# Performance work log

Hardware: AMD Instinct MI355X
Metric: run time of the kernel (lower is better)

## Reference

```python
import jax, jax.numpy as jnp
import numpy as np

B, T, C = 4, 1024, 1024
HS = 64                 # head_size_a
H = C // HS             # 16 heads
H_KV = 4                # num_key_value_heads
N_REP = H // H_KV       # GQA repeat factor
D_DECAY = 64            # max(32, round(1.8*sqrt(1024)/32)*32)
D_MV = 32               # max(32, round(1.3*sqrt(1024)/32)*32)
LAYER_ID = 1
N_LAYER = 24
EPS = 0.00064


def setup_inputs() -> dict:
    key = jax.random.key(0)
    ks = jax.random.split(key, 16)
    def nrm(k, shape, s):
        return jax.random.normal(k, shape, jnp.float32) * s
    ratio_0_to_1 = LAYER_ID / (N_LAYER - 1)
    n = np.arange(C, dtype=np.float64)
    decay_speed = -7.0 + 5.0 * (n / (C - 1)) ** (0.85 + 1.0 * ratio_0_to_1 ** 0.5)
    return dict(
        x=nrm(ks[0], (B, T, C), 1.0),
        v_first=nrm(ks[1], (B, T, C), 1.0),
        attention_mask=jnp.ones((B, T), jnp.float32),
        Wr=nrm(ks[2], (H * HS, C), C ** -0.5),
        Wk=nrm(ks[3], (H_KV * HS, C), C ** -0.5),
        Wv=nrm(ks[4], (H_KV * HS, C), C ** -0.5),
        Wo=nrm(ks[5], (C, H * HS), C ** -0.5),
        w0=jnp.asarray(decay_speed + 0.5, jnp.float32),
        w1=nrm(ks[6], (C, D_DECAY), 0.02),
        w2=nrm(ks[7], (D_DECAY, C), 0.02),
        a0=jnp.zeros((C,), jnp.float32),
        a1=nrm(ks[8], (C, D_DECAY), 0.02),
        a2=nrm(ks[9], (D_DECAY, C), 0.02),
        v0=jnp.ones((C,), jnp.float32),
        v1=nrm(ks[10], (C, D_MV), 0.02),
        v2=nrm(ks[11], (D_MV, C), 0.02),
        k_k=jnp.full((C,), 0.85, jnp.float32),
        k_a=jnp.ones((C,), jnp.float32),
        r_k=nrm(ks[12], (H, HS), 0.02),
        ln_g=jnp.ones((C,), jnp.float32),
        ln_b=jnp.zeros((C,), jnp.float32),
    )


def _wkv7(r, w, k, v, a, b, mask):
    """RWKV-7 delta-rule recurrence. r,w,k,v,a,b: (B,T,C); mask: (B,T).
    State S: (B,H,N_value,N_key). Per step:
      S = S * exp(-exp(w)) + (S @ a) b^T + v k^T ;  y = S @ r
    """
    Bx, Tx, Cx = r.shape
    def rs(t):  # (B,T,C) -> (T,B,H,N)
        return t.reshape(Bx, Tx, H, HS).transpose(1, 0, 2, 3)
    decay = jnp.exp(-jnp.exp(w))
    m = mask.T[:, :, None, None]  # (T,B,1,1)
    rT, dT, kT, vT, aT, bT = map(rs, (r, decay, k, v, a, b))
    kT = kT * m; vT = vT * m; aT = aT * m; bT = bT * m
    dT = jnp.where(m > 0, dT, 1.0)  # masked steps leave state untouched

    def step(S, inp):
        r_t, d_t, k_t, v_t, a_t, b_t = inp  # each (B,H,N)
        sa = jnp.einsum('bhij,bhj->bhi', S, a_t)
        S = S * d_t[:, :, None, :] + sa[..., None] * b_t[:, :, None, :] \
            + v_t[..., None] * k_t[:, :, None, :]
        y = jnp.einsum('bhij,bhj->bhi', S, r_t)
        return S, y

    S0 = jnp.zeros((Bx, H, HS, HS), r.dtype)
    _, yT = jax.lax.scan(step, S0, (rT, dT, kT, vT, aT, bT))
    return yT.transpose(1, 0, 2, 3).reshape(Bx, Tx, Cx)


def reference(x, v_first, attention_mask, Wr, Wk, Wv, Wo, w0, w1, w2,
              a0, a1, a2, v0, v1, v2, k_k, k_a, r_k, ln_g, ln_b):
    B_, T_, C_ = x.shape
    r = x @ Wr.T
    w = -jax.nn.softplus(-(w0 + jnp.tanh(x @ w1) @ w2)) - 0.6
    k = x @ Wk.T  # (B,T,H_KV*HS)
    v = x @ Wv.T

    def rep(t):  # GQA repeat_kv: (B,T,H_kv*N) -> (B,T,H*N)
        t = t.reshape(B_, T_, H_KV, 1, HS)
        return jnp.broadcast_to(t, (B_, T_, H_KV, N_REP, HS)).reshape(B_, T_, C_)
    k = rep(k); v = rep(v)

    # layer_id != 0: residual mix with first layer's v
    v = v + (v_first - v) * jax.nn.sigmoid(v0 + x @ v1 @ v2)
    a = jax.nn.sigmoid(a0 + x @ a1 @ a2)

    kk = (k * k_k).reshape(B_, T_, H, HS)
    kk = kk / jnp.maximum(jnp.linalg.norm(kk, axis=-1, keepdims=True), 1e-12)
    kk = kk.reshape(B_, T_, C_)
    k = k * (1.0 + (a - 1.0) * k_a)

    y = _wkv7(r, w, k, v, -kk, kk * a, attention_mask)

    # GroupNorm(H, C): per-head normalization over HS channels
    yh = y.reshape(B_, T_, H, HS)
    mu = yh.mean(-1, keepdims=True)
    var = yh.var(-1, keepdims=True)
    y = ((yh - mu) / jnp.sqrt(var + EPS)).reshape(B_, T_, C_) * ln_g + ln_b

    rk = (r.reshape(B_, T_, H, HS) * k.reshape(B_, T_, H, HS) * r_k).sum(-1, keepdims=True)
    y = y + (rk * v.reshape(B_, T_, H, HS)).reshape(B_, T_, C_)
    out = y @ Wo.T
    return (out, v_first)
```

## Files before the change

### kernel.cpp

```cpp
#include <hip/hip_runtime.h>


#define NROWS 4096
#define CCH   1024
#define EPSV  0.00064f

typedef __attribute__((ext_vector_type(4))) float f32x4;
typedef __attribute__((ext_vector_type(8))) short bf16x8;

__device__ __forceinline__ unsigned short f2b(float f) {
    unsigned x = __float_as_uint(f);
    return (unsigned short)((x + 0x7fffu + ((x >> 16) & 1u)) >> 16);
}
__device__ __forceinline__ float b2f(unsigned short u) {
    return __uint_as_float(((unsigned)u) << 16);
}

#define LDSTR 40

template<bool TANH>
__global__ __launch_bounds__(256) void gemm_split(
    const float* __restrict__ A, int lda, const float* __restrict__ B, int ldb,
    float* __restrict__ C, int ldc, int M, int N, int K, int tl, int th)
{
    __shared__ __align__(16) unsigned short Ah[128 * LDSTR];
    __shared__ __align__(16) unsigned short Al[128 * LDSTR];
    __shared__ __align__(16) unsigned short Bh[128 * LDSTR];
    __shared__ __align__(16) unsigned short Bl[128 * LDSTR];
    const int t = threadIdx.x;
    const int wave = t >> 6, lane = t & 63;
    const int m0 = blockIdx.y * 128, n0 = blockIdx.x * 128;
    const int wm = (wave >> 1) * 64, wn = (wave & 1) * 64;
    const int fr = lane & 15, kq = lane >> 4;

    f32x4 acc[4][4];
    #pragma unroll
    for (int i = 0; i < 4; ++i)
        #pragma unroll
        for (int j = 0; j < 4; ++j)
            acc[i][j] = (f32x4){0.f, 0.f, 0.f, 0.f};

    const int srow = t >> 3;
    const int scol = (t & 7) * 4;

    for (int k0 = 0; k0 < K; k0 += 32) {
        #pragma unroll
        for (int p = 0; p < 4; ++p) {
            const int row = p * 32 + srow;
            {
                const float4 v = *reinterpret_cast<const float4*>(
                    A + (size_t)(m0 + row) * lda + k0 + scol);
                ushort4 h, l;
                h.x = f2b(v.x); l.x = f2b(v.x - b2f(h.x));
                h.y = f2b(v.y); l.y = f2b(v.y - b2f(h.y));
                h.z = f2b(v.z); l.z = f2b(v.z - b2f(h.z));
                h.w = f2b(v.w); l.w = f2b(v.w - b2f(h.w));
                *reinterpret_cast<ushort4*>(&Ah[row * LDSTR + scol]) = h;
                *reinterpret_cast<ushort4*>(&Al[row * LDSTR + scol]) = l;
            }
            {
                float4 v = make_float4(0.f, 0.f, 0.f, 0.f);
                if (n0 + row < N)
                    v = *reinterpret_cast<const float4*>(
                        B + (size_t)(n0 + row) * ldb + k0 + scol);
                ushort4 h, l;
                h.x = f2b(v.x); l.x = f2b(v.x - b2f(h.x));
                h.y = f2b(v.y); l.y = f2b(v.y - b2f(h.y));
                h.z = f2b(v.z); l.z = f2b(v.z - b2f(h.z));
                h.w = f2b(v.w); l.w = f2b(v.w - b2f(h.w));
                *reinterpret_cast<ushort4*>(&Bh[row * LDSTR + scol]) = h;
                *reinterpret_cast<ushort4*>(&Bl[row * LDSTR + scol]) = l;
            }
        }
        __syncthreads();

        bf16x8 ah[4], al[4], bh[4], bl[4];
        #pragma unroll
        for (int mi = 0; mi < 4; ++mi) {
            ah[mi] = *reinterpret_cast<const bf16x8*>(&Ah[(wm + mi * 16 + fr) * LDSTR + kq * 8]);
            al[mi] = *reinterpret_cast<const bf16x8*>(&Al[(wm + mi * 16 + fr) * LDSTR + kq * 8]);
        }
        #pragma unroll
        for (int ni = 0; ni < 4; ++ni) {
            bh[ni] = *reinterpret_cast<const bf16x8*>(&Bh[(wn + ni * 16 + fr) * LDSTR + kq * 8]);
            bl[ni] = *reinterpret_cast<const bf16x8*>(&Bl[(wn + ni * 16 + fr) * LDSTR + kq * 8]);
        }
        #pragma unroll
        for (int mi = 0; mi < 4; ++mi)
            #pragma unroll
            for (int ni = 0; ni < 4; ++ni) {
                acc[mi][ni] = __builtin_amdgcn_mfma_f32_16x16x32_bf16(
                    al[mi], bh[ni], acc[mi][ni], 0, 0, 0);
                acc[mi][ni] = __builtin_amdgcn_mfma_f32_16x16x32_bf16(
                    ah[mi], bl[ni], acc[mi][ni], 0, 0, 0);
                acc[mi][ni] = __builtin_amdgcn_mfma_f32_16x16x32_bf16(
                    ah[mi], bh[ni], acc[mi][ni], 0, 0, 0);
            }
        __syncthreads();
    }

    const int crow0 = m0 + wm + kq * 4;
    const int ccol0 = n0 + wn + fr;
    #pragma unroll
    for (int mi = 0; mi < 4; ++mi)
        #pragma unroll
        for (int ni = 0; ni < 4; ++ni) {
            const int col = ccol0 + ni * 16;
            if (col < N) {
                #pragma unroll
                for (int i = 0; i < 4; ++i) {
                    float v = acc[mi][ni][i];
                    if (TANH && col >= tl && col < th) v = tanhf(v);
                    C[(size_t)(crow0 + mi * 16 + i) * ldc + col] = v;
                }
            }
        }
}

__global__ __launch_bounds__(256) void gemm_mfma(
    const float* __restrict__ A, int lda, const float* __restrict__ B, int ldb,
    float* __restrict__ C, int ldc, int M, int N, int K)
{
    __shared__ __align__(16) unsigned short Ah[128 * LDSTR];
    __shared__ __align__(16) unsigned short Bh[128 * LDSTR];
    const int t = threadIdx.x;
    const int wave = t >> 6, lane = t & 63;
    const int m0 = blockIdx.y * 128, n0 = blockIdx.x * 128;
    const int wm = (wave >> 1) * 64, wn = (wave & 1) * 64;
    const int fr = lane & 15, kq = lane >> 4;

    f32x4 acc[4][4];
    #pragma unroll
    for (int i = 0; i < 4; ++i)
        #pragma unroll
        for (int j = 0; j < 4; ++j)
            acc[i][j] = (f32x4){0.f, 0.f, 0.f, 0.f};

    const int srow = t >> 3;
    const int scol = (t & 7) * 4;

    for (int k0 = 0; k0 < K; k0 += 32) {
        #pragma unroll
        for (int p = 0; p < 4; ++p) {
            const int row = p * 32 + srow;
            const float4 av = *reinterpret_cast<const float4*>(
                A + (size_t)(m0 + row) * lda + k0 + scol);
            ushort4 a4;
            a4.x = f2b(av.x); a4.y = f2b(av.y); a4.z = f2b(av.z); a4.w = f2b(av.w);
            *reinterpret_cast<ushort4*>(&Ah[row * LDSTR + scol]) = a4;
            const float4 bv = *reinterpret_cast<const float4*>(
                B + (size_t)(n0 + row) * ldb + k0 + scol);
            ushort4 b4;
            b4.x = f2b(bv.x); b4.y = f2b(bv.y); b4.z = f2b(bv.z); b4.w = f2b(bv.w);
            *reinterpret_cast<ushort4*>(&Bh[row * LDSTR + scol]) = b4;
        }
        __syncthreads();

        bf16x8 af[4], bfr[4];
        #pragma unroll
        for (int mi = 0; mi < 4; ++mi)
            af[mi] = *reinterpret_cast<const bf16x8*>(&Ah[(wm + mi * 16 + fr) * LDSTR + kq * 8]);
        #pragma unroll
        for (int ni = 0; ni < 4; ++ni)
            bfr[ni] = *reinterpret_cast<const bf16x8*>(&Bh[(wn + ni * 16 + fr) * LDSTR + kq * 8]);
        #pragma unroll
        for (int mi = 0; mi < 4; ++mi)
            #pragma unroll
            for (int ni = 0; ni < 4; ++ni)
                acc[mi][ni] = __builtin_amdgcn_mfma_f32_16x16x32_bf16(
                    af[mi], bfr[ni], acc[mi][ni], 0, 0, 0);
        __syncthreads();
    }

    const int crow0 = m0 + wm + kq * 4;
    const int ccol0 = n0 + wn + fr;
    #pragma unroll
    for (int mi = 0; mi < 4; ++mi)
        #pragma unroll
        for (int ni = 0; ni < 4; ++ni) {
            const int col = ccol0 + ni * 16;
            #pragma unroll
            for (int i = 0; i < 4; ++i)
                C[(size_t)(crow0 + mi * 16 + i) * ldc + col] = acc[mi][ni][i];
        }
}

__global__ __launch_bounds__(256) void gemm_stage2(
    const float* __restrict__ kvh,
    const float* __restrict__ w2T, const float* __restrict__ a2T,
    const float* __restrict__ v2T,
    float* __restrict__ wdec, float* __restrict__ kf, float* __restrict__ vf)
{
    const int z = blockIdx.z;
    const float* A = kvh + (z == 0 ? 512 : z == 1 ? 576 : 640);
    const float* B = z == 0 ? w2T : z == 1 ? a2T : v2T;
    float* C       = z == 0 ? wdec : z == 1 ? kf : vf;
    const int K    = z == 2 ? 32 : 64;
    const int ldb  = K;

    __shared__ __align__(16) unsigned short Ah[128 * LDSTR];
    __shared__ __align__(16) unsigned short Bh[128 * LDSTR];
    const int t = threadIdx.x;
    const int wave = t >> 6, lane = t & 63;
    const int m0 = blockIdx.y * 128, n0 = blockIdx.x * 128;
    const int wm = (wave >> 1) * 64, wn = (wave & 1) * 64;
    const int fr = lane & 15, kq = lane >> 4;

    f32x4 acc[4][4];
    #pragma unroll
    for (int i = 0; i < 4; ++i)
        #pragma unroll
        for (int j = 0; j < 4; ++j)
            acc[i][j] = (f32x4){0.f, 0.f, 0.f, 0.f};

    const int srow = t >> 3;
    const int scol = (t & 7) * 4;

    for (int k0 = 0; k0 < K; k0 += 32) {
        #pragma unroll
        for (int p = 0; p < 4; ++p) {
            const int row = p * 32 + srow;
            const float4 av = *reinterpret_cast<const float4*>(
                A + (size_t)(m0 + row) * 672 + k0 + scol);
            ushort4 a4;
            a4.x = f2b(av.x); a4.y = f2b(av.y); a4.z = f2b(av.z); a4.w = f2b(av.w);
            *reinterpret_cast<ushort4*>(&Ah[row * LDSTR + scol]) = a4;
            const float4 bv = *reinterpret_cast<const float4*>(
                B + (size_t)(n0 + row) * ldb + k0 + scol);
            ushort4 b4;
            b4.x = f2b(bv.x); b4.y = f2b(bv.y); b4.z = f2b(bv.z); b4.w = f2b(bv.w);
            *reinterpret_cast<ushort4*>(&Bh[row * LDSTR + scol]) = b4;
        }
        __syncthreads();

        bf16x8 af[4], bfr[4];
        #pragma unroll
        for (int mi = 0; mi < 4; ++mi)
            af[mi] = *reinterpret_cast<const bf16x8*>(&Ah[(wm + mi * 16 + fr) * LDSTR + kq * 8]);
        #pragma unroll
        for (int ni = 0; ni < 4; ++ni)
            bfr[ni] = *reinterpret_cast<const bf16x8*>(&Bh[(wn + ni * 16 + fr) * LDSTR + kq * 8]);
        #pragma unroll
        for (int mi = 0; mi < 4; ++mi)
            #pragma unroll
            for (int ni = 0; ni < 4; ++ni)
                acc[mi][ni] = __builtin_amdgcn_mfma_f32_16x16x32_bf16(
                    af[mi], bfr[ni], acc[mi][ni], 0, 0, 0);
        __syncthreads();
    }

    const int crow0 = m0 + wm + kq * 4;
    const int ccol0 = n0 + wn + fr;
    #pragma unroll
    for (int mi = 0; mi < 4; ++mi)
        #pragma unroll
        for (int ni = 0; ni < 4; ++ni) {
            const int col = ccol0 + ni * 16;
            #pragma unroll
            for (int i = 0; i < 4; ++i)
                C[(size_t)(crow0 + mi * 16 + i) * 1024 + col] = acc[mi][ni][i];
        }
}

__global__ __launch_bounds__(256) void pack_all(
    const float* __restrict__ Wk, const float* __restrict__ Wv,
    const float* __restrict__ w1, const float* __restrict__ a1,
    const float* __restrict__ v1, const float* __restrict__ w2,
    const float* __restrict__ a2, const float* __restrict__ v2,
    float* __restrict__ Wkvh,
    float* __restrict__ w2T, float* __restrict__ a2T, float* __restrict__ v2T)
{
    const int blk = blockIdx.x, t = threadIdx.x;
    if (blk < 512) {
        const float* s = blk < 256 ? Wk + (size_t)blk * 1024
                                   : Wv + (size_t)(blk - 256) * 1024;
        const float4 v = *reinterpret_cast<const float4*>(s + t * 4);
        *reinterpret_cast<float4*>(Wkvh + (size_t)blk * 1024 + t * 4) = v;
    } else if (blk < 672) {
        const int f = blk - 512;
        for (int c = t; c < 1024; c += 256) {
            float val;
            if (f < 64)       val = w1[c * 64 + f];
            else if (f < 128) val = a1[c * 64 + (f - 64)];
            else              val = v1[c * 32 + (f - 128)];
            Wkvh[(size_t)(512 + f) * 1024 + c] = val;
        }
    } else {
        const int c = blk - 672;
        if (t < 64)       w2T[c * 64 + t]         = w2[t * 1024 + c];
        else if (t < 128) a2T[c * 64 + (t - 64)]  = a2[(t - 64) * 1024 + c];
        else if (t < 160) v2T[c * 32 + (t - 128)] = v2[(t - 128) * 1024 + c];
    }
}

__global__ __launch_bounds__(256) void fuse_pre(
    const float* __restrict__ kvh,
    const float* __restrict__ v_first, const float* __restrict__ mask,
    const float* __restrict__ w0, const float* __restrict__ a0,
    const float* __restrict__ v0,
    const float* __restrict__ k_k, const float* __restrict__ k_a,
    float* __restrict__ wdec, float* __restrict__ kf, float* __restrict__ vf,
    float* __restrict__ aab, float* __restrict__ bbb)
{
    const int n = blockIdx.x, t = threadIdx.x;
    const float m = mask[n];
    const bool live = m > 0.f;

    #pragma unroll
    for (int q = 0; q < 4; ++q) {
        const int c = q * 256 + t;
        const size_t idx = (size_t)n * 1024 + c;
        const float dd   = w0[c] + wdec[idx];
        const float aacc = a0[c] + kf[idx];
        const float vacc = v0[c] + vf[idx];

        const float u  = -dd;
        const float sp = fmaxf(u, 0.f) + log1pf(expf(-fabsf(u)));
        const float dec = expf(-expf(-sp - 0.6f));
        const float av = 1.f / (1.f + expf(-aacc));
        const float sv = 1.f / (1.f + expf(-vacc));

        const int  ck  = q * 64 + (c & 63);
        const float kr = kvh[(size_t)n * 672 + ck];
        const float vr = kvh[(size_t)n * 672 + 256 + ck];
        const float vfi = v_first[idx];
        const float vv  = vr + (vfi - vr) * sv;

        const float tkk = kr * k_k[c];
        float ss = tkk * tkk;
        #pragma unroll
        for (int off = 32; off > 0; off >>= 1) ss += __shfl_xor(ss, off, 64);
        const float kkv = tkk / fmaxf(sqrtf(ss), 1e-12f);

        wdec[idx] = live ? dec : 1.f;
        kf[idx]   = kr * (1.f + (av - 1.f) * k_a[c]) * m;
        vf[idx]   = vv * m;
        aab[idx]  = -kkv * m;
        bbb[idx]  = kkv * av * m;
    }
}

__device__ __forceinline__ float qred16(float x) {
    x += __int_as_float(__builtin_amdgcn_update_dpp(
        0, __float_as_int(x), 0xB1, 0xF, 0xF, true));
    x += __int_as_float(__builtin_amdgcn_update_dpp(
        0, __float_as_int(x), 0x4E, 0xF, 0xF, true));
    x += __int_as_float(__builtin_amdgcn_update_dpp(
        0, __float_as_int(x), 0x141, 0xF, 0xF, true));
    x += __int_as_float(__builtin_amdgcn_update_dpp(
        0, __float_as_int(x), 0x140, 0xF, 0xF, true));
    return x;
}

__global__ __launch_bounds__(256, 1) void wkv7(
    const float* __restrict__ r, const float* __restrict__ wdec,
    const float* __restrict__ kf, const float* __restrict__ vf,
    const float* __restrict__ aab, const float* __restrict__ bbb,
    float* __restrict__ y)
{
    __shared__ __align__(16) float4 sl[2][672];
    const int blk = blockIdx.x;
    const int m  = blk & 7;
    const int s_ = blk >> 3;
    const int bh = (s_ >> 2) * 8 + m;
    const int j  = s_ & 3;
    const int b = bh >> 4, h = bh & 15;
    const int tid  = threadIdx.x;
    const int wave = tid >> 6;
    const int lane = tid & 63;
    const int li   = lane & 15;
    const int il   = wave * 4 + (lane >> 4);
    const int i    = j * 16 + il;
    const size_t cb = (size_t)b * (1024 * 1024) + (size_t)h * 64;

#define GLL16(g, l) __builtin_amdgcn_global_load_lds( \
        (const __attribute__((address_space(1))) unsigned int*)(g), \
        (__attribute__((address_space(3))) unsigned int*)(l), 16, 0, 0)

    auto stage = [&](int t0, int bf) {
        #pragma unroll
        for (int k = 0; k < 3; ++k) {
            const int q = tid + k * 256;
            if (q < 672) {
                const float* gp;
                if (q < 640) {
                    const int s  = q / 80;
                    const int rm = q - s * 80;
                    const int arr = rm >> 4, c16 = rm & 15;
                    const float* base = arr == 0 ? wdec : arr == 1 ? kf
                                      : arr == 2 ? aab : arr == 3 ? bbb : r;
                    gp = base + cb + (size_t)(t0 + s) * 1024 + c16 * 4;
                } else {
                    const int qq = q - 640;
                    const int s = qq >> 2, c4 = qq & 3;
                    gp = vf + cb + (size_t)(t0 + s) * 1024 + j * 16 + c4 * 4;
                }
                GLL16(gp, &sl[bf][wave * 64 + k * 256]);
            }
        }
    };

    float4 S = (float4){0.f, 0.f, 0.f, 0.f};

    stage(0, 0);
    asm volatile("s_waitcnt vmcnt(0)" ::: "memory");
    __builtin_amdgcn_sched_barrier(0);
    __builtin_amdgcn_s_barrier();

    for (int g = 0; g < 128; ++g) {
        const int bf = g & 1;
        const int t0 = g * 8;
        if (g + 1 < 128) stage(t0 + 8, bf ^ 1);
        __builtin_amdgcn_sched_barrier(0);

        #pragma unroll
        for (int s = 0; s < 8; ++s) {
            const float4 d4 = sl[bf][s * 80 + 0  + li];
            const float4 k4 = sl[bf][s * 80 + 16 + li];
            const float4 a4 = sl[bf][s * 80 + 32 + li];
            const float4 b4 = sl[bf][s * 80 + 48 + li];
            const float4 r4 = sl[bf][s * 80 + 64 + li];
            const float  vv = reinterpret_cast<const float*>(
                                  &sl[bf][640 + s * 4])[il];

            float sa = S.x * a4.x + S.y * a4.y + S.z * a4.z + S.w * a4.w;
            sa = qred16(sa);
            S.x = S.x * d4.x + sa * b4.x + vv * k4.x;
            S.y = S.y * d4.y + sa * b4.y + vv * k4.y;
            S.z = S.z * d4.z + sa * b4.z + vv * k4.z;
            S.w = S.w * d4.w + sa * b4.w + vv * k4.w;
            float yv = S.x * r4.x + S.y * r4.y + S.z * r4.z + S.w * r4.w;
            yv = qred16(yv);
            if (li == 0) y[cb + (size_t)(t0 + s) * 1024 + i] = yv;
        }

        asm volatile("s_waitcnt vmcnt(8)" ::: "memory");
        __builtin_amdgcn_sched_barrier(0);
        __builtin_amdgcn_s_barrier();
    }
#undef GLL16
}

__global__ __launch_bounds__(256) void fuse_post(
    const float* __restrict__ y, const float* __restrict__ r,
    const float* __restrict__ kf, const float* __restrict__ vf,
    const float* __restrict__ r_k, const float* __restrict__ ln_g, const float* __restrict__ ln_b,
    float* __restrict__ yn)
{
    const int n = blockIdx.x, t = threadIdx.x;
    #pragma unroll
    for (int q = 0; q < 4; ++q) {
        const int c = q * 256 + t;
        const size_t idx = (size_t)n * 1024 + c;
        const float yv = y[idx];
        float s1 = yv, s2 = yv * yv;
        float rk = r[idx] * kf[idx] * r_k[c];
        #pragma unroll
        for (int off = 32; off > 0; off >>= 1) {
            s1 += __shfl_xor(s1, off, 64);
            s2 += __shfl_xor(s2, off, 64);
            rk += __shfl_xor(rk, off, 64);
        }
        const float mu  = s1 * (1.f / 64.f);
        const float var = s2 * (1.f / 64.f) - mu * mu;
        yn[idx] = (yv - mu) * rsqrtf(var + EPSV) * ln_g[c] + ln_b[c]
                  + rk * vf[idx];
    }
}

extern "C" void kernel_launch(void* const* d_in, const int* in_sizes, int n_in,
                              void* d_out, int out_size, void* d_ws, size_t ws_size,
                              hipStream_t stream)
{
    const float* x       = (const float*)d_in[0];
    const float* v_first = (const float*)d_in[1];
    const float* mask    = (const float*)d_in[2];
    const float* Wr      = (const float*)d_in[3];
    const float* Wk      = (const float*)d_in[4];
    const float* Wv      = (const float*)d_in[5];
    const float* Wo      = (const float*)d_in[6];
    const float* w0      = (const float*)d_in[7];
    const float* w1      = (const float*)d_in[8];
    const float* w2      = (const float*)d_in[9];
    const float* a0      = (const float*)d_in[10];
    const float* a1      = (const float*)d_in[11];
    const float* a2      = (const float*)d_in[12];
    const float* v0      = (const float*)d_in[13];
    const float* v1      = (const float*)d_in[14];
    const float* v2      = (const float*)d_in[15];
    const float* k_k     = (const float*)d_in[16];
    const float* k_a     = (const float*)d_in[17];
    const float* r_k     = (const float*)d_in[18];
    const float* ln_g    = (const float*)d_in[19];
    const float* ln_b    = (const float*)d_in[20];
    float* out = (float*)d_out;

    float* ws = (float*)d_ws;
    const size_t M4 = (size_t)NROWS * CCH;
    float* rbuf = ws;
    float* wdec = ws + 1 * M4;
    float* kf   = ws + 2 * M4;
    float* vf   = ws + 3 * M4;
    float* aab  = ws + 4 * M4;
    float* bbb  = ws + 5 * M4;
    float* ybuf = ws + 6 * M4;
    float* kvh  = ybuf;
    float* w2T  = kvh  + (size_t)NROWS * 672;
    float* a2T  = w2T  + (size_t)1024 * 64;
    float* v2T  = a2T  + (size_t)1024 * 64;
    float* Wkvh = v2T  + (size_t)1024 * 32;
    float* yn = aab;

    dim3 blk(256);
    pack_all<<<1696, blk, 0, stream>>>(Wk, Wv, w1, a1, v1, w2, a2, v2,
                                       Wkvh, w2T, a2T, v2T);
    gemm_mfma<<<dim3(8, 32), blk, 0, stream>>>(
        x, 1024, Wr, 1024, rbuf, 1024, NROWS, 1024, 1024);
    gemm_split<true><<<dim3(6, 32), blk, 0, stream>>>(
        x, 1024, Wkvh, 1024, kvh, 672, NROWS, 672, 1024, 512, 576);
    gemm_stage2<<<dim3(8, 32, 3), blk, 0, stream>>>(
        kvh, w2T, a2T, v2T, wdec, kf, vf);
    fuse_pre<<<NROWS, blk, 0, stream>>>(kvh, v_first, mask, w0, a0, v0,
                                        k_k, k_a, wdec, kf, vf, aab, bbb);
    wkv7<<<256, blk, 0, stream>>>(rbuf, wdec, kf, vf, aab, bbb, ybuf);
    fuse_post<<<NROWS, blk, 0, stream>>>(ybuf, rbuf, kf, vf, r_k, ln_g, ln_b, yn);
    gemm_mfma<<<dim3(8, 32), blk, 0, stream>>>(
        yn, 1024, Wo, 1024, out, 1024, NROWS, 1024, 1024);
    hipMemcpyAsync(out + M4, v_first, M4 * sizeof(float),
                   hipMemcpyDeviceToDevice, stream);
}
```

Measured before the change: 492.5 us.

## Split WKV7 state rows across twice as many blocks with 32-lane reductions

The recurrence kernel now gives each block 8 value rows of a head instead of 16, and launches 512 blocks instead of 256. Each lane holds 2 state elements instead of 4, and the dot-product reductions span 32 lanes by adding a cross-row shuffle after the DPP steps. The aim is more parallelism and shorter per-step arithmetic on the serial time chain. In exchange, every block still stages the full key-side vectors, so global and LDS traffic rises, and each step gains extra shuffle latency.

```diff
diff --git a/kernel.cpp b/kernel.cpp
--- a/kernel.cpp
+++ b/kernel.cpp
@@ -340,7 +340,7 @@
     }
 }
 
-__device__ __forceinline__ float qred16(float x) {
+__device__ __forceinline__ float red32(float x) {
     x += __int_as_float(__builtin_amdgcn_update_dpp(
         0, __float_as_int(x), 0xB1, 0xF, 0xF, true));
     x += __int_as_float(__builtin_amdgcn_update_dpp(
@@ -349,6 +349,7 @@
         0, __float_as_int(x), 0x141, 0xF, 0xF, true));
     x += __int_as_float(__builtin_amdgcn_update_dpp(
         0, __float_as_int(x), 0x140, 0xF, 0xF, true));
+    x += __shfl_xor(x, 16, 32);
     return x;
 }
 
@@ -358,19 +359,19 @@
     const float* __restrict__ aab, const float* __restrict__ bbb,
     float* __restrict__ y)
 {
-    __shared__ __align__(16) float4 sl[2][672];
+    __shared__ __align__(16) float4 sl[2][656];
     const int blk = blockIdx.x;
     const int m  = blk & 7;
-    const int s_ = blk >> 3;
-    const int bh = (s_ >> 2) * 8 + m;
-    const int j  = s_ & 3;
+    const int g_ = blk >> 3;
+    const int bh = (g_ >> 3) * 8 + m;
+    const int u  = g_ & 7;
     const int b = bh >> 4, h = bh & 15;
     const int tid  = threadIdx.x;
     const int wave = tid >> 6;
     const int lane = tid & 63;
-    const int li   = lane & 15;
-    const int il   = wave * 4 + (lane >> 4);
-    const int i    = j * 16 + il;
+    const int jl   = lane & 31;
+    const int il   = wave * 2 + (lane >> 5);
+    const int i    = u * 8 + il;
     const size_t cb = (size_t)b * (1024 * 1024) + (size_t)h * 64;
 
 #define GLL16(g, l) __builtin_amdgcn_global_load_lds( \
@@ -381,7 +382,7 @@
         #pragma unroll
         for (int k = 0; k < 3; ++k) {
             const int q = tid + k * 256;
-            if (q < 672) {
+            if (q < 656) {
                 const float* gp;
                 if (q < 640) {
                     const int s  = q / 80;
@@ -392,15 +393,15 @@
                     gp = base + cb + (size_t)(t0 + s) * 1024 + c16 * 4;
                 } else {
                     const int qq = q - 640;
-                    const int s = qq >> 2, c4 = qq & 3;
-                    gp = vf + cb + (size_t)(t0 + s) * 1024 + j * 16 + c4 * 4;
+                    const int s = qq >> 1, c4 = qq & 1;
+                    gp = vf + cb + (size_t)(t0 + s) * 1024 + u * 8 + c4 * 4;
                 }
                 GLL16(gp, &sl[bf][wave * 64 + k * 256]);
             }
         }
     };
 
-    float4 S = (float4){0.f, 0.f, 0.f, 0.f};
+    float2 S = make_float2(0.f, 0.f);
 
     stage(0, 0);
     asm volatile("s_waitcnt vmcnt(0)" ::: "memory");
@@ -415,23 +416,20 @@
 
         #pragma unroll
         for (int s = 0; s < 8; ++s) {
-            const float4 d4 = sl[bf][s * 80 + 0  + li];
-            const float4 k4 = sl[bf][s * 80 + 16 + li];
-            const float4 a4 = sl[bf][s * 80 + 32 + li];
-            const float4 b4 = sl[bf][s * 80 + 48 + li];
-            const float4 r4 = sl[bf][s * 80 + 64 + li];
-            const float  vv = reinterpret_cast<const float*>(
-                                  &sl[bf][640 + s * 4])[il];
-
-            float sa = S.x * a4.x + S.y * a4.y + S.z * a4.z + S.w * a4.w;
-            sa = qred16(sa);
-            S.x = S.x * d4.x + sa * b4.x + vv * k4.x;
-            S.y = S.y * d4.y + sa * b4.y + vv * k4.y;
-            S.z = S.z * d4.z + sa * b4.z + vv * k4.z;
-            S.w = S.w * d4.w + sa * b4.w + vv * k4.w;
-            float yv = S.x * r4.x + S.y * r4.y + S.z * r4.z + S.w * r4.w;
-            yv = qred16(yv);
-            if (li == 0) y[cb + (size_t)(t0 + s) * 1024 + i] = yv;
+            const float2 d2 = reinterpret_cast<const float2*>(&sl[bf][s * 80 + 0 ])[jl];
+            const float2 k2 = reinterpret_cast<const float2*>(&sl[bf][s * 80 + 16])[jl];
+            const float2 a2 = reinterpret_cast<const float2*>(&sl[bf][s * 80 + 32])[jl];
+            const float2 b2 = reinterpret_cast<const float2*>(&sl[bf][s * 80 + 48])[jl];
+            const float2 r2 = reinterpret_cast<const float2*>(&sl[bf][s * 80 + 64])[jl];
+            const float  vv = reinterpret_cast<const float*>(&sl[bf][640 + s * 2])[il];
+
+            float sa = S.x * a2.x + S.y * a2.y;
+            sa = red32(sa);
+            S.x = S.x * d2.x + sa * b2.x + vv * k2.x;
+            S.y = S.y * d2.y + sa * b2.y + vv * k2.y;
+            float yv = S.x * r2.x + S.y * r2.y;
+            yv = red32(yv);
+            if (jl == 0) y[cb + (size_t)(t0 + s) * 1024 + i] = yv;
         }
 
         asm volatile("s_waitcnt vmcnt(8)" ::: "memory");
@@ -522,7 +520,7 @@
         kvh, w2T, a2T, v2T, wdec, kf, vf);
     fuse_pre<<<NROWS, blk, 0, stream>>>(kvh, v_first, mask, w0, a0, v0,
                                         k_k, k_a, wdec, kf, vf, aab, bbb);
-    wkv7<<<256, blk, 0, stream>>>(rbuf, wdec, kf, vf, aab, bbb, ybuf);
+    wkv7<<<512, blk, 0, stream>>>(rbuf, wdec, kf, vf, aab, bbb, ybuf);
     fuse_post<<<NROWS, blk, 0, stream>>>(ybuf, rbuf, kf, vf, r_k, ln_g, ln_b, yn);
     gemm_mfma<<<dim3(8, 32), blk, 0, stream>>>(
         yn, 1024, Wo, 1024, out, 1024, NROWS, 1024, 1024);
```

After: 543.7 us. 1.1x slower.
